# Performance work log

Measured on AMD Instinct MI355X. Metric: run time of the kernel, lower is better.

Reference implementation:

```python
import jax, jax.numpy as jnp
import numpy as np


def setup_inputs() -> dict:
    key = jax.random.key(0)
    x = jax.random.normal(key, (8192, 4096), dtype=jnp.float32)
    return {"x": x}


def reference(x) -> jnp.ndarray:
    # Sparsemax along the last axis (dim=-1), matching the torch module's math.
    n = x.shape[-1]
    x = x - jnp.max(x, axis=-1, keepdims=True)
    # sort descending
    zs = jnp.flip(jnp.sort(x, axis=-1), axis=-1)  # [B, N]
    r = jnp.arange(1, n + 1, dtype=x.dtype)       # [N]
    bound = 1.0 + r * zs
    cum_zs = jnp.cumsum(zs, axis=-1)
    is_gt = (bound > cum_zs).astype(x.dtype)
    k = jnp.max(is_gt * r, axis=-1, keepdims=True)          # support size
    taus = (jnp.sum(is_gt * zs, axis=-1, keepdims=True) - 1.0) / k
    return jnp.maximum(jnp.zeros_like(x), x - taus)
```

## Files before the change

### kernel.cpp

```cpp
#include <hip/hip_runtime.h>


#define COLS 4096
#define WAVES_PER_BLOCK 4
#define MAX_NEWTON_ITERS 16

__global__ __launch_bounds__(256) void sparsemax_kernel(
    const float* __restrict__ x, float* __restrict__ out, int rows) {
  const int lane = threadIdx.x & 63;
  const int wid = threadIdx.x >> 6;
  const long row = (long)blockIdx.x * WAVES_PER_BLOCK + wid;
  if (row >= rows) return;

  const float4* __restrict__ xr =
      reinterpret_cast<const float4*>(x + row * COLS);
  float4* __restrict__ outr = reinterpret_cast<float4*>(out + row * COLS);

  float4 v[16];
#pragma unroll
  for (int j = 0; j < 16; ++j) v[j] = xr[lane + j * 64];

#pragma unroll
  for (int j = 0; j < 16; ++j) {
    asm volatile("" : "+v"(v[j].x), "+v"(v[j].y), "+v"(v[j].z), "+v"(v[j].w));
  }

  float m = fmaxf(fmaxf(v[0].x, v[0].y), fmaxf(v[0].z, v[0].w));
#pragma unroll
  for (int j = 1; j < 16; ++j) {
    m = fmaxf(m, fmaxf(fmaxf(v[j].x, v[j].y), fmaxf(v[j].z, v[j].w)));
  }
#pragma unroll
  for (int off = 32; off > 0; off >>= 1) m = fmaxf(m, __shfl_xor(m, off));

  float tau = m - 1.0f;

  for (int it = 0; it < MAX_NEWTON_ITERS; ++it) {
    float s = 0.0f;
    int c = 0;
#pragma unroll
    for (int j = 0; j < 16; ++j) {
      s += (v[j].x > tau) ? v[j].x : 0.0f;
      c += (v[j].x > tau) ? 1 : 0;
      s += (v[j].y > tau) ? v[j].y : 0.0f;
      c += (v[j].y > tau) ? 1 : 0;
      s += (v[j].z > tau) ? v[j].z : 0.0f;
      c += (v[j].z > tau) ? 1 : 0;
      s += (v[j].w > tau) ? v[j].w : 0.0f;
      c += (v[j].w > tau) ? 1 : 0;
    }
#pragma unroll
    for (int off = 32; off > 0; off >>= 1) {
      s += __shfl_xor(s, off);
      c += __shfl_xor(c, off);
    }
    float ntau = (s - 1.0f) / (float)c;
    if (ntau == tau) break;
    tau = ntau;
  }

#pragma unroll
  for (int j = 0; j < 16; ++j) {
    float4 o;
    o.x = fmaxf(v[j].x - tau, 0.0f);
    o.y = fmaxf(v[j].y - tau, 0.0f);
    o.z = fmaxf(v[j].z - tau, 0.0f);
    o.w = fmaxf(v[j].w - tau, 0.0f);
    outr[lane + j * 64] = o;
  }
}

extern "C" void kernel_launch(void* const* d_in, const int* in_sizes, int n_in,
                              void* d_out, int out_size, void* d_ws,
                              size_t ws_size, hipStream_t stream) {
  const float* x = (const float*)d_in[0];
  float* out = (float*)d_out;
  const int rows = in_sizes[0] / COLS;
  const int blocks = (rows + WAVES_PER_BLOCK - 1) / WAVES_PER_BLOCK;
  sparsemax_kernel<<<blocks, 256, 0, stream>>>(x, out, rows);
}
```

Baseline: 234.8 us.

## Stage rows in LDS and iterate Newton solve on compacted candidate list

The row is now kept in shared memory instead of 64 float4 registers per lane. Elements above max-1 are compacted into a small per-wave candidate buffer using LDS atomics, and the Newton iteration for tau runs only over those candidates, falling back to the full row if the buffer overflows. The aim is to cut the per-iteration work from 4096 elements to the few hundred that can be in the support. In exchange it uses about 80KB of LDS per block, which limits occupancy, and the compaction adds per-element shared atomics.

```diff
diff --git a/kernel.cpp b/kernel.cpp
--- a/kernel.cpp
+++ b/kernel.cpp
@@ -3,69 +3,99 @@
 
 #define COLS 4096
 #define WAVES_PER_BLOCK 4
-#define MAX_NEWTON_ITERS 16
+#define CAND_CAP 960
+#define MAX_ITERS 32
 
 __global__ __launch_bounds__(256) void sparsemax_kernel(
     const float* __restrict__ x, float* __restrict__ out, int rows) {
+  __shared__ __align__(16) float rowbuf[WAVES_PER_BLOCK][COLS];
+  __shared__ __align__(16) float cand[WAVES_PER_BLOCK][CAND_CAP];
+  __shared__ int cnt[WAVES_PER_BLOCK];
+
   const int lane = threadIdx.x & 63;
   const int wid = threadIdx.x >> 6;
   const long row = (long)blockIdx.x * WAVES_PER_BLOCK + wid;
   if (row >= rows) return;
 
+  if (lane == 0) cnt[wid] = 0;
+
   const float4* __restrict__ xr =
       reinterpret_cast<const float4*>(x + row * COLS);
   float4* __restrict__ outr = reinterpret_cast<float4*>(out + row * COLS);
+  float4* rb = reinterpret_cast<float4*>(rowbuf[wid]);
 
-  float4 v[16];
-#pragma unroll
-  for (int j = 0; j < 16; ++j) v[j] = xr[lane + j * 64];
-
+  float m = -INFINITY;
 #pragma unroll
   for (int j = 0; j < 16; ++j) {
-    asm volatile("" : "+v"(v[j].x), "+v"(v[j].y), "+v"(v[j].z), "+v"(v[j].w));
-  }
-
-  float m = fmaxf(fmaxf(v[0].x, v[0].y), fmaxf(v[0].z, v[0].w));
-#pragma unroll
-  for (int j = 1; j < 16; ++j) {
-    m = fmaxf(m, fmaxf(fmaxf(v[j].x, v[j].y), fmaxf(v[j].z, v[j].w)));
+    float4 v = xr[lane + j * 64];
+    rb[lane + j * 64] = v;
+    m = fmaxf(m, fmaxf(fmaxf(v.x, v.y), fmaxf(v.z, v.w)));
   }
 #pragma unroll
   for (int off = 32; off > 0; off >>= 1) m = fmaxf(m, __shfl_xor(m, off));
 
-  float tau = m - 1.0f;
+  const float thr = m - 1.0f;
 
-  for (int it = 0; it < MAX_NEWTON_ITERS; ++it) {
-    float s = 0.0f;
-    int c = 0;
 #pragma unroll
-    for (int j = 0; j < 16; ++j) {
-      s += (v[j].x > tau) ? v[j].x : 0.0f;
-      c += (v[j].x > tau) ? 1 : 0;
-      s += (v[j].y > tau) ? v[j].y : 0.0f;
-      c += (v[j].y > tau) ? 1 : 0;
-      s += (v[j].z > tau) ? v[j].z : 0.0f;
-      c += (v[j].z > tau) ? 1 : 0;
-      s += (v[j].w > tau) ? v[j].w : 0.0f;
-      c += (v[j].w > tau) ? 1 : 0;
+  for (int j = 0; j < 16; ++j) {
+    float4 v = rb[lane + j * 64];
+    if (v.x > thr) { int p = atomicAdd(&cnt[wid], 1); if (p < CAND_CAP) cand[wid][p] = v.x; }
+    if (v.y > thr) { int p = atomicAdd(&cnt[wid], 1); if (p < CAND_CAP) cand[wid][p] = v.y; }
+    if (v.z > thr) { int p = atomicAdd(&cnt[wid], 1); if (p < CAND_CAP) cand[wid][p] = v.z; }
+    if (v.w > thr) { int p = atomicAdd(&cnt[wid], 1); if (p < CAND_CAP) cand[wid][p] = v.w; }
+  }
+
+  const int nc = cnt[wid];
+  float tau = thr;
+
+  if (nc <= CAND_CAP) {
+    for (int it = 0; it < MAX_ITERS; ++it) {
+      float s = 0.0f;
+      int c = 0;
+      for (int k = lane; k < nc; k += 64) {
+        float v = cand[wid][k];
+        if (v > tau) { s += v; c += 1; }
+      }
+#pragma unroll
+      for (int off = 32; off > 0; off >>= 1) {
+        s += __shfl_xor(s, off);
+        c += __shfl_xor(c, off);
+      }
+      float ntau = (s - 1.0f) / (float)c;
+      if (ntau == tau) break;
+      tau = ntau;
     }
+  } else {
+    for (int it = 0; it < MAX_ITERS; ++it) {
+      float s = 0.0f;
+      int c = 0;
 #pragma unroll
-    for (int off = 32; off > 0; off >>= 1) {
-      s += __shfl_xor(s, off);
-      c += __shfl_xor(c, off);
+      for (int j = 0; j < 16; ++j) {
+        float4 v = rb[lane + j * 64];
+        if (v.x > tau) { s += v.x; c += 1; }
+        if (v.y > tau) { s += v.y; c += 1; }
+        if (v.z > tau) { s += v.z; c += 1; }
+        if (v.w > tau) { s += v.w; c += 1; }
+      }
+#pragma unroll
+      for (int off = 32; off > 0; off >>= 1) {
+        s += __shfl_xor(s, off);
+        c += __shfl_xor(c, off);
+      }
+      float ntau = (s - 1.0f) / (float)c;
+      if (ntau == tau) break;
+      tau = ntau;
     }
-    float ntau = (s - 1.0f) / (float)c;
-    if (ntau == tau) break;
-    tau = ntau;
   }
 
 #pragma unroll
   for (int j = 0; j < 16; ++j) {
+    float4 v = rb[lane + j * 64];
     float4 o;
-    o.x = fmaxf(v[j].x - tau, 0.0f);
-    o.y = fmaxf(v[j].y - tau, 0.0f);
-    o.z = fmaxf(v[j].z - tau, 0.0f);
-    o.w = fmaxf(v[j].w - tau, 0.0f);
+    o.x = fmaxf(v.x - tau, 0.0f);
+    o.y = fmaxf(v.y - tau, 0.0f);
+    o.z = fmaxf(v.z - tau, 0.0f);
+    o.w = fmaxf(v.w - tau, 0.0f);
     outr[lane + j * 64] = o;
   }
 }
```

Measured after the change: 232.6 us. Within noise of the previous version (-0.9%).
